# Optimization experiments

Measured on AMD Instinct MI355X. Metric: run time of the kernel, lower is better.

## Reference

```python
import jax, jax.numpy as jnp
import numpy as np

F = 16          # features
C = 128         # context features
H = 256         # conditioner hidden
L = 8           # coupling layers
K = 8           # spline bins
TB = 3.0        # tail bound
T = F // 2      # transform features per layer (8)
PDIM = 3 * K - 1  # params per transformed feature (23), tails='linear'
MIN_W = MIN_H = MIN_D = 1e-3
B = 65536


def _feature_split(layer):
    ev = np.arange(0, F, 2)
    od = np.arange(1, F, 2)
    tr, idn = (ev, od) if layer % 2 == 0 else (od, ev)  # mask>0 => transform
    inv = np.argsort(np.concatenate([idn, tr]))
    return idn, tr, inv


def _rq_spline(x, uw, uh, ud):
    """Monotonic rational-quadratic spline with linear tails (nflows semantics).
    x: [B,T]; uw/uh: [B,T,K]; ud: [B,T,K-1]. Returns (y, logabsdet) per element."""
    const = np.log(np.expm1(1.0 - MIN_D))  # pad value so boundary derivative == 1
    ud = jnp.pad(ud, ((0, 0), (0, 0), (1, 1)), constant_values=const)  # [B,T,K+1]
    inside = (x >= -TB) & (x <= TB)
    xs = jnp.clip(x, -TB, TB)

    w = jax.nn.softmax(uw, axis=-1)
    w = MIN_W + (1.0 - MIN_W * K) * w
    cw = jnp.pad(jnp.cumsum(w, -1), ((0, 0), (0, 0), (1, 0)))
    cw = 2.0 * TB * cw - TB
    cw = cw.at[..., 0].set(-TB).at[..., -1].set(TB)
    w = cw[..., 1:] - cw[..., :-1]

    d = MIN_D + jax.nn.softplus(ud)  # [B,T,K+1]

    h = jax.nn.softmax(uh, axis=-1)
    h = MIN_H + (1.0 - MIN_H * K) * h
    ch = jnp.pad(jnp.cumsum(h, -1), ((0, 0), (0, 0), (1, 0)))
    ch = 2.0 * TB * ch - TB
    ch = ch.at[..., 0].set(-TB).at[..., -1].set(TB)
    h = ch[..., 1:] - ch[..., :-1]

    # bin search on cumulative widths (forward direction)
    idx = jnp.clip(jnp.sum((xs[..., None] >= cw).astype(jnp.int32), -1) - 1, 0, K - 1)
    g = lambda a: jnp.take_along_axis(a, idx[..., None], axis=-1)[..., 0]

    x0, bw = g(cw[..., :K]), g(w)
    y0, bh = g(ch[..., :K]), g(h)
    delta = g(h / w)
    d0, d1 = g(d[..., :K]), g(d[..., 1:])

    th = (xs - x0) / bw
    th1m = th * (1.0 - th)
    num = bh * (delta * th * th + d0 * th1m)
    den = delta + (d0 + d1 - 2.0 * delta) * th1m
    y = y0 + num / den
    dnum = delta * delta * (d1 * th * th + 2.0 * delta * th1m + d0 * (1.0 - th) ** 2)
    ld = jnp.log(dnum) - 2.0 * jnp.log(den)
    return jnp.where(inside, y, x), jnp.where(inside, ld, 0.0)


def setup_inputs() -> dict:
    key = jax.random.key(0)
    ks = jax.random.split(key, 8)
    inputs = jax.random.normal(ks[0], (B, F), jnp.float32)
    context = jax.random.normal(ks[1], (B, C), jnp.float32)
    s = lambda k, shape, fan: jax.random.normal(k, shape, jnp.float32) / np.sqrt(fan)
    W1 = s(ks[2], (L, T + C, H), T + C)
    b1 = jnp.zeros((L, H), jnp.float32)
    W2 = s(ks[3], (L, H, H), H)
    b2 = jnp.zeros((L, H), jnp.float32)
    W3 = s(ks[4], (L, H, T * PDIM), H)
    b3 = jnp.zeros((L, T * PDIM), jnp.float32)
    rng = np.random.default_rng(0)  # fixed-at-init RandomPermutation buffers
    perms = jnp.asarray(np.stack([rng.permutation(F) for _ in range(L - 1)]), jnp.int32)
    return dict(inputs=inputs, context=context, W1=W1, b1=b1, W2=W2, b2=b2,
                W3=W3, b3=b3, perms=perms)


def reference(inputs, context, W1, b1, W2, b2, W3, b3, perms):
    x = jnp.clip(inputs, -1.0, 1.0)
    logdet = jnp.zeros(x.shape[0], x.dtype)
    for i in range(L):
        idn, tr, inv = _feature_split(i)
        xi = x[:, idn]
        xt = x[:, tr]
        hdn = jax.nn.relu(jnp.concatenate([xi, context], -1) @ W1[i] + b1[i])
        hdn = jax.nn.relu(hdn @ W2[i] + b2[i])
        p = (hdn @ W3[i] + b3[i]).reshape(-1, T, PDIM)
        yt, ld = _rq_spline(xt, p[..., :K], p[..., K:2 * K], p[..., 2 * K:])
        x = jnp.concatenate([xi, yt], -1)[:, inv]
        logdet = logdet + jnp.sum(ld, -1)
        if i < L - 1:
            x = x[:, perms[i]]
    return jnp.clip(x, -1.0, 1.0), logdet
```

## Files before the change

kernel.cpp:

```cpp
#include <hip/hip_runtime.h>
#include <math.h>

#define BATCH 65536
#define FDIM 16
#define CDIM 128
#define HDIM 256
#define NL 8
#define KBINS 8
#define TDIM 8
#define PD 23
#define TBV 3.0f
#define K1 160
#define N3 184
#define N3P 192
#define PSTR 197
#define MR 64
#define XSTR 40

typedef _Float16 f16;
typedef __attribute__((ext_vector_type(8))) _Float16 f16x8;
typedef __attribute__((ext_vector_type(4))) float f32x4;

__global__ __launch_bounds__(256)
void conv_w1_kernel(const float* __restrict__ W1,
                    f16* __restrict__ Wh, f16* __restrict__ Wl) {
    int idx = blockIdx.x * 256 + threadIdx.x;
    if (idx >= NL * HDIM * K1) return;
    int l = idx / (HDIM * K1);
    int rem = idx - l * (HDIM * K1);
    int n = rem / K1;
    int k = rem - n * K1;
    int row = (k < 128) ? (8 + k) : ((k < 136) ? (k - 128) : -1);
    float v = (row >= 0) ? W1[((size_t)l * 136 + row) * HDIM + n] : 0.f;
    f16 hv = (f16)v;
    Wh[idx] = hv; Wl[idx] = (f16)(v - (float)hv);
}

__global__ __launch_bounds__(256)
void conv_w2_kernel(const float* __restrict__ W2,
                    f16* __restrict__ Wh, f16* __restrict__ Wl) {
    int idx = blockIdx.x * 256 + threadIdx.x;
    if (idx >= NL * HDIM * HDIM) return;
    int l = idx / (HDIM * HDIM);
    int rem = idx - l * (HDIM * HDIM);
    int n = rem >> 8;
    int k = rem & 255;
    float v = W2[((size_t)l * HDIM + k) * HDIM + n];
    f16 hv = (f16)v;
    Wh[idx] = hv; Wl[idx] = (f16)(v - (float)hv);
}

__global__ __launch_bounds__(256)
void conv_w3_kernel(const float* __restrict__ W3,
                    f16* __restrict__ Wh, f16* __restrict__ Wl) {
    int idx = blockIdx.x * 256 + threadIdx.x;
    if (idx >= NL * N3P * HDIM) return;
    int l = idx / (N3P * HDIM);
    int rem = idx - l * (N3P * HDIM);
    int n = rem >> 8;
    int k = rem & 255;
    float v = (n < N3) ? W3[((size_t)l * HDIM + k) * N3 + n] : 0.f;
    f16 hv = (f16)v;
    Wh[idx] = hv; Wl[idx] = (f16)(v - (float)hv);
}

__global__ __launch_bounds__(256)
void conv_ctx_kernel(const float* __restrict__ ctx,
                     f16* __restrict__ ch, f16* __restrict__ cl) {
    size_t idx = ((size_t)blockIdx.x * 256 + threadIdx.x) * 4;
    if (idx >= (size_t)BATCH * CDIM) return;
    float4 v = *(const float4*)&ctx[idx];
    f16 h;
    h = (f16)v.x; ch[idx + 0] = h; cl[idx + 0] = (f16)(v.x - (float)h);
    h = (f16)v.y; ch[idx + 1] = h; cl[idx + 1] = (f16)(v.y - (float)h);
    h = (f16)v.z; ch[idx + 2] = h; cl[idx + 2] = (f16)(v.z - (float)h);
    h = (f16)v.w; ch[idx + 3] = h; cl[idx + 3] = (f16)(v.w - (float)h);
}

__device__ __forceinline__ float softplusf(float v) {
    return fmaxf(v, 0.f) + log1pf(expf(-fabsf(v)));
}

__device__ __forceinline__ void gld16(const f16* src, f16* dst) {
    __builtin_amdgcn_global_load_lds(
        (const __attribute__((address_space(1))) unsigned int*)src,
        (__attribute__((address_space(3))) unsigned int*)dst, 16, 0, 0);
}

template<int N> __device__ __forceinline__ void vmw() {
    asm volatile("s_waitcnt vmcnt(%0)" :: "n"(N) : "memory");
}
__device__ __forceinline__ void barr() {
    __builtin_amdgcn_s_barrier();
    __builtin_amdgcn_sched_barrier(0);
}
__device__ __forceinline__ void lgkm_bar() {
    asm volatile("s_waitcnt lgkmcnt(0)" ::: "memory");
    __builtin_amdgcn_s_barrier();
    __builtin_amdgcn_sched_barrier(0);
}

__global__ __launch_bounds__(512, 1)
void flow_kernel(const float* __restrict__ in,
                 const f16* __restrict__ ctxh, const f16* __restrict__ ctxl,
                 const f16* __restrict__ W1h, const f16* __restrict__ W1l,
                 const f16* __restrict__ W2h, const f16* __restrict__ W2l,
                 const f16* __restrict__ W3h, const f16* __restrict__ W3l,
                 const float* __restrict__ b1, const float* __restrict__ b2,
                 const float* __restrict__ b3, const int* __restrict__ perms,
                 float* __restrict__ out) {
    __shared__ __align__(16) char arena[131072];
    __shared__ __align__(16) f16 sXi[2][MR * XSTR];
    __shared__ float sX[2][MR][17];
    __shared__ float sY[MR][9];
    __shared__ float sLd[MR][9];
    __shared__ float sLdet[MR];
    __shared__ float sBias[768];
    __shared__ int   sPerm[(NL - 1) * FDIM];

    f16* sH = (f16*)arena;
    float* sP = (float*)arena;

    const int tid = threadIdx.x;
    const int lane = tid & 63;
    const int w = tid >> 6;
    const int lr = lane & 15, lh = lane >> 4;
    const int bid = blockIdx.x;
    const int wgid = (bid & 7) * 32 + (bid >> 3);
    const int wcol0 = w * 32;
    const int bxor = (lh ^ (lr & 3)) << 4;

    char* const wbuf = arena + 32768 + w * 12288;

    auto stageB = [&](const f16* Wh, const f16* Wl, int b, int kt, int KD) {
        char* dst = wbuf + b * 4096;
        #pragma unroll
        for (int ii = 0; ii < 2; ++ii) {
            int si = ii * 64 + lane;
            int c = si >> 2, seg = si & 3;
            const f16* sh = Wh + (size_t)(wcol0 + c) * KD + kt * 32 + (seg ^ (c & 3)) * 8;
            const f16* sl = Wl + (size_t)(wcol0 + c) * KD + kt * 32 + (seg ^ (c & 3)) * 8;
            gld16(sh, (f16*)(dst + ii * 1024 + lane * 16));
            gld16(sl, (f16*)(dst + 2048 + ii * 1024 + lane * 16));
        }
    };

    for (int rb = 0; rb < 4; ++rb) {
        const int rbase = (rb * 256 + wgid) * MR;
        lgkm_bar();

        {
            int r = tid >> 3, c2 = (tid & 7) * 2;
            float2 v = *(const float2*)&in[(size_t)(rbase + r) * FDIM + c2];
            sX[0][r][c2 + 0] = fminf(fmaxf(v.x, -1.f), 1.f);
            sX[0][r][c2 + 1] = fminf(fmaxf(v.y, -1.f), 1.f);
        }
        if (tid < MR) sLdet[tid] = 0.f;
        if (rb == 0 && tid < (NL - 1) * FDIM) sPerm[tid] = perms[tid];

        int cur = 0;
        for (int l = 0; l < NL; ++l) {
            lgkm_bar();

            {
                float bv1 = (tid < 256) ? b1[l * HDIM + tid]
                                        : b2[l * HDIM + (tid - 256)];
                float bv3 = b3[l * N3 + (tid < N3 ? tid : N3 - 1)];
                sBias[tid] = bv1;
                if (tid < N3) sBias[512 + tid] = bv3;
            }
            if (tid < MR) {
                int r = tid, off = 1 - (l & 1);
                #pragma unroll
                for (int k = 0; k < 8; ++k) {
                    float v = sX[cur][r][2 * k + off];
                    f16 hv = (f16)v;
                    sXi[0][r * XSTR + k] = hv;
                    sXi[1][r * XSTR + k] = (f16)(v - (float)hv);
                }
                #pragma unroll
                for (int k = 8; k < 32; ++k) {
                    sXi[0][r * XSTR + k] = (f16)0.f;
                    sXi[1][r * XSTR + k] = (f16)0.f;
                }
            }
            #pragma unroll
            for (int s = 0; s < 4; ++s) {
                int slot = s * 512 + tid;
                int p = slot >> 10, sp = slot & 1023;
                int row = sp >> 4, blk = sp & 15;
                const f16* src = (p ? ctxl : ctxh)
                               + (size_t)(rbase + row) * CDIM + (blk ^ (row & 7)) * 8;
                gld16(src, (f16*)(arena + slot * 16));
            }
            const f16* W1hL = W1h + (size_t)l * HDIM * K1;
            const f16* W1lL = W1l + (size_t)l * HDIM * K1;
            const f16* W2hL = W2h + (size_t)l * HDIM * HDIM;
            const f16* W2lL = W2l + (size_t)l * HDIM * HDIM;
            const f16* W3hL = W3h + (size_t)l * N3P * HDIM;
            const f16* W3lL = W3l + (size_t)l * N3P * HDIM;
            stageB(W1hL, W1lL, 0, 0, K1);
            stageB(W1hL, W1lL, 1, 1, K1);
            vmw<8>();
            lgkm_bar();

            f32x4 acc[4][2];
            #pragma unroll
            for (int i = 0; i < 4; ++i)
                #pragma unroll
                for (int j = 0; j < 2; ++j) acc[i][j] = (f32x4){0.f, 0.f, 0.f, 0.f};
            #pragma unroll
            for (int kt = 0; kt < 5; ++kt) {
                if (kt < 3) stageB(W1hL, W1lL, (kt + 2) % 3, kt + 2, K1);
                if (kt < 3) vmw<8>(); else if (kt == 3) vmw<4>(); else vmw<0>();
                f16x8 ah[4], al[4];
                if (kt < 4) {
                    #pragma unroll
                    for (int i = 0; i < 4; ++i) {
                        int row = i * 16 + lr;
                        int byo = row * 256 + ((kt * 64 + lh * 16) ^ ((row & 7) << 4));
                        ah[i] = *(const f16x8*)(arena + byo);
                        al[i] = *(const f16x8*)(arena + 16384 + byo);
                    }
                } else {
                    #pragma unroll
                    for (int i = 0; i < 4; ++i) {
                        int row = i * 16 + lr;
                        ah[i] = *(const f16x8*)&sXi[0][row * XSTR + lh * 8];
                        al[i] = *(const f16x8*)&sXi[1][row * XSTR + lh * 8];
                    }
                }
                const char* bb = wbuf + (kt % 3) * 4096;
                __builtin_amdgcn_s_setprio(1);
                #pragma unroll
                for (int j = 0; j < 2; ++j) {
                    int cb = (j * 16 + lr) * 64 + bxor;
                    f16x8 bh = *(const f16x8*)(bb + cb);
                    f16x8 bl = *(const f16x8*)(bb + 2048 + cb);
                    #pragma unroll
                    for (int i = 0; i < 4; ++i) {
                        acc[i][j] = __builtin_amdgcn_mfma_f32_16x16x32_f16(ah[i], bh, acc[i][j], 0, 0, 0);
                        acc[i][j] = __builtin_amdgcn_mfma_f32_16x16x32_f16(ah[i], bl, acc[i][j], 0, 0, 0);
                        acc[i][j] = __builtin_amdgcn_mfma_f32_16x16x32_f16(al[i], bh, acc[i][j], 0, 0, 0);
                    }
                }
                __builtin_amdgcn_s_setprio(0);
            }
            barr();
            #pragma unroll
            for (int j = 0; j < 2; ++j) {
                int col = wcol0 + j * 16 + lr;
                float bv = sBias[col];
                #pragma unroll
                for (int i = 0; i < 4; ++i)
                    #pragma unroll
                    for (int q = 0; q < 4; ++q) {
                        float v = fmaxf(acc[i][j][q] + bv, 0.f);
                        int row = i * 16 + lh * 4 + q;
                        int e = ((row << 8) + col) ^ ((row & 7) << 3);
                        sH[e] = (f16)v;
                    }
            }
            stageB(W2hL, W2lL, 0, 0, HDIM);
            stageB(W2hL, W2lL, 1, 1, HDIM);
            lgkm_bar();

            #pragma unroll
            for (int i = 0; i < 4; ++i)
                #pragma unroll
                for (int j = 0; j < 2; ++j) acc[i][j] = (f32x4){0.f, 0.f, 0.f, 0.f};
            #pragma unroll
            for (int kt = 0; kt < 8; ++kt) {
                if (kt < 6) stageB(W2hL, W2lL, (kt + 2) % 3, kt + 2, HDIM);
                if (kt < 6) vmw<8>(); else if (kt == 6) vmw<4>(); else vmw<0>();
                int k0 = kt * 32 + lh * 8;
                f16x8 ah[4];
                #pragma unroll
                for (int i = 0; i < 4; ++i) {
                    int row = i * 16 + lr;
                    int e = ((row << 8) + k0) ^ ((row & 7) << 3);
                    ah[i] = *(const f16x8*)&sH[e];
                }
                const char* bb = wbuf + (kt % 3) * 4096;
                __builtin_amdgcn_s_setprio(1);
                #pragma unroll
                for (int j = 0; j < 2; ++j) {
                    int cb = (j * 16 + lr) * 64 + bxor;
                    f16x8 bh = *(const f16x8*)(bb + cb);
                    f16x8 bl = *(const f16x8*)(bb + 2048 + cb);
                    #pragma unroll
                    for (int i = 0; i < 4; ++i) {
                        acc[i][j] = __builtin_amdgcn_mfma_f32_16x16x32_f16(ah[i], bh, acc[i][j], 0, 0, 0);
                        acc[i][j] = __builtin_amdgcn_mfma_f32_16x16x32_f16(ah[i], bl, acc[i][j], 0, 0, 0);
                    }
                }
                __builtin_amdgcn_s_setprio(0);
            }
            barr();
            #pragma unroll
            for (int j = 0; j < 2; ++j) {
                int col = wcol0 + j * 16 + lr;
                float bv = sBias[256 + col];
                #pragma unroll
                for (int i = 0; i < 4; ++i)
                    #pragma unroll
                    for (int q = 0; q < 4; ++q) {
                        float v = fmaxf(acc[i][j][q] + bv, 0.f);
                        int row = i * 16 + lh * 4 + q;
                        int e = ((row << 8) + col) ^ ((row & 7) << 3);
                        sH[e] = (f16)v;
                    }
            }
            if (w < 6) {
                stageB(W3hL, W3lL, 0, 0, HDIM);
                stageB(W3hL, W3lL, 1, 1, HDIM);
            }
            lgkm_bar();

            f32x4 acc3[4][2];
            #pragma unroll
            for (int i = 0; i < 4; ++i)
                #pragma unroll
                for (int j = 0; j < 2; ++j) acc3[i][j] = (f32x4){0.f, 0.f, 0.f, 0.f};
            if (w < 6) {
                #pragma unroll
                for (int kt = 0; kt < 8; ++kt) {
                    if (kt < 6) stageB(W3hL, W3lL, (kt + 2) % 3, kt + 2, HDIM);
                    if (kt < 6) vmw<8>(); else if (kt == 6) vmw<4>(); else vmw<0>();
                    int k0 = kt * 32 + lh * 8;
                    f16x8 ah[4];
                    #pragma unroll
                    for (int i = 0; i < 4; ++i) {
                        int row = i * 16 + lr;
                        int e = ((row << 8) + k0) ^ ((row & 7) << 3);
                        ah[i] = *(const f16x8*)&sH[e];
                    }
                    const char* bb = wbuf + (kt % 3) * 4096;
                    __builtin_amdgcn_s_setprio(1);
                    #pragma unroll
                    for (int j = 0; j < 2; ++j) {
                        int cb = (j * 16 + lr) * 64 + bxor;
                        f16x8 bh = *(const f16x8*)(bb + cb);
                        f16x8 bl = *(const f16x8*)(bb + 2048 + cb);
                        #pragma unroll
                        for (int i = 0; i < 4; ++i) {
                            acc3[i][j] = __builtin_amdgcn_mfma_f32_16x16x32_f16(ah[i], bh, acc3[i][j], 0, 0, 0);
                            acc3[i][j] = __builtin_amdgcn_mfma_f32_16x16x32_f16(ah[i], bl, acc3[i][j], 0, 0, 0);
                        }
                    }
                    __builtin_amdgcn_s_setprio(0);
                }
            }
            barr();
            if (w < 6) {
                #pragma unroll
                for (int j = 0; j < 2; ++j) {
                    int col = wcol0 + j * 16 + lr;
                    float bv = (col < N3) ? sBias[512 + col] : 0.f;
                    #pragma unroll
                    for (int i = 0; i < 4; ++i)
                        #pragma unroll
                        for (int q = 0; q < 4; ++q) {
                            int row = i * 16 + lh * 4 + q;
                            sP[row * PSTR + col] = acc3[i][j][q] + bv;
                        }
                }
            }
            lgkm_bar();

            {
                int r = tid & 63, t = tid >> 6;
                float xin = sX[cur][r][2 * t + (l & 1)];
                const float* pp = &sP[r * PSTR + t * PD];
                bool inside = (xin >= -TBV) && (xin <= TBV);
                float xs = fminf(fmaxf(xin, -TBV), TBV);

                float e0, e1, e2, e3, e4, e5, e6, e7;
                {
                    float a0 = pp[0], a1 = pp[1], a2 = pp[2], a3 = pp[3];
                    float a4 = pp[4], a5 = pp[5], a6 = pp[6], a7 = pp[7];
                    float m = fmaxf(fmaxf(fmaxf(a0, a1), fmaxf(a2, a3)),
                                    fmaxf(fmaxf(a4, a5), fmaxf(a6, a7)));
                    e0 = expf(a0 - m); e1 = expf(a1 - m); e2 = expf(a2 - m); e3 = expf(a3 - m);
                    e4 = expf(a4 - m); e5 = expf(a5 - m); e6 = expf(a6 - m); e7 = expf(a7 - m);
                }
                float swv = ((e0 + e1) + (e2 + e3)) + ((e4 + e5) + (e6 + e7));
                float cwc = (1.f - 0.001f * KBINS) / swv;
                float x0 = -TBV, x1 = TBV;
                int idx = 0;
                bool done = false;
                {
                    float cs = 0.f;
                    float ee[7] = {e0, e1, e2, e3, e4, e5, e6};
                    #pragma unroll
                    for (int k = 0; k < 7; ++k) {
                        cs += 0.001f + cwc * ee[k];
                        float nxt = 2.f * TBV * cs - TBV;
                        bool ge = (xs >= nxt);
                        x0 = ge ? nxt : x0;
                        idx += ge ? 1 : 0;
                        x1 = (!ge && !done) ? nxt : x1;
                        done = done || !ge;
                    }
                }
                float y0 = -TBV, y1 = TBV;
                {
                    float a0 = pp[8], a1 = pp[9], a2 = pp[10], a3 = pp[11];
                    float a4 = pp[12], a5 = pp[13], a6 = pp[14], a7 = pp[15];
                    float m = fmaxf(fmaxf(fmaxf(a0, a1), fmaxf(a2, a3)),
                                    fmaxf(fmaxf(a4, a5), fmaxf(a6, a7)));
                    float f0 = expf(a0 - m), f1 = expf(a1 - m), f2 = expf(a2 - m), f3 = expf(a3 - m);
                    float f4 = expf(a4 - m), f5 = expf(a5 - m), f6 = expf(a6 - m), f7 = expf(a7 - m);
                    float shv = ((f0 + f1) + (f2 + f3)) + ((f4 + f5) + (f6 + f7));
                    float chc = (1.f - 0.001f * KBINS) / shv;
                    float cs = 0.f;
                    float ff[7] = {f0, f1, f2, f3, f4, f5, f6};
                    #pragma unroll
                    for (int k = 0; k < 7; ++k) {
                        cs += 0.001f + chc * ff[k];
                        float nxt = 2.f * TBV * cs - TBV;
                        y0 = (k < idx) ? nxt : y0;
                        y1 = (k == idx) ? nxt : y1;
                    }
                }
                float udm = pp[16 + (idx > 0 ? idx - 1 : 0)];
                float udp = pp[16 + (idx < 7 ? idx : 6)];
                float d0 = (idx > 0) ? 0.001f + softplusf(udm) : 1.f;
                float d1 = (idx < 7) ? 0.001f + softplusf(udp) : 1.f;

                float bw = x1 - x0, bh2 = y1 - y0;
                float delta = bh2 / bw;
                float th = (xs - x0) / bw;
                float th1m = th * (1.f - th);
                float num = bh2 * (delta * th * th + d0 * th1m);
                float den = delta + (d0 + d1 - 2.f * delta) * th1m;
                float y = y0 + num / den;
                float omth = 1.f - th;
                float dnum = delta * delta * (d1 * th * th + 2.f * delta * th1m + d0 * omth * omth);
                float ldv = logf(dnum) - 2.f * logf(den);
                sY[r][t] = inside ? y : xin;
                sLd[r][t] = inside ? ldv : 0.f;
            }
            lgkm_bar();

            {
                int r = tid >> 3, f0 = (tid & 7) * 2;
                if (l < NL - 1) {
                    #pragma unroll
                    for (int ff = 0; ff < 2; ++ff) {
                        int f = f0 + ff;
                        int g = sPerm[l * FDIM + f];
                        float v = ((g & 1) == (l & 1)) ? sY[r][g >> 1] : sX[cur][r][g];
                        sX[cur ^ 1][r][f] = v;
                    }
                    if (f0 == 0) {
                        float s = 0.f;
                        #pragma unroll
                        for (int t = 0; t < 8; ++t) s += sLd[r][t];
                        sLdet[r] += s;
                    }
                } else {
                    float ov[2];
                    #pragma unroll
                    for (int ff = 0; ff < 2; ++ff) {
                        int f = f0 + ff;
                        float v = ((f & 1) == (l & 1)) ? sY[r][f >> 1] : sX[cur][r][f];
                        ov[ff] = fminf(fmaxf(v, -1.f), 1.f);
                    }
                    float2 o = {ov[0], ov[1]};
                    *(float2*)&out[(size_t)(rbase + r) * FDIM + f0] = o;
                    if (f0 == 0) {
                        float s = 0.f;
                        #pragma unroll
                        for (int t = 0; t < 8; ++t) s += sLd[r][t];
                        out[(size_t)BATCH * FDIM + rbase + r] = sLdet[r] + s;
                    }
                }
            }
            cur ^= 1;
        }
    }
}

extern "C" void kernel_launch(void* const* d_in, const int* in_sizes, int n_in,
                              void* d_out, int out_size, void* d_ws, size_t ws_size,
                              hipStream_t stream) {
    (void)in_sizes; (void)n_in; (void)out_size; (void)ws_size;
    const float* inputs  = (const float*)d_in[0];
    const float* context = (const float*)d_in[1];
    const float* W1 = (const float*)d_in[2];
    const float* b1 = (const float*)d_in[3];
    const float* W2 = (const float*)d_in[4];
    const float* b2 = (const float*)d_in[5];
    const float* W3 = (const float*)d_in[6];
    const float* b3 = (const float*)d_in[7];
    const int*   perms = (const int*)d_in[8];
    float* out = (float*)d_out;

    f16* W1h = (f16*)d_ws;
    f16* W1l = W1h + (size_t)NL * HDIM * K1;
    f16* W2h = W1l + (size_t)NL * HDIM * K1;
    f16* W2l = W2h + (size_t)NL * HDIM * HDIM;
    f16* W3h = W2l + (size_t)NL * HDIM * HDIM;
    f16* W3l = W3h + (size_t)NL * N3P * HDIM;
    f16* ctxh = W3l + (size_t)NL * N3P * HDIM;
    f16* ctxl = ctxh + (size_t)BATCH * CDIM;

    int n1 = NL * HDIM * K1;
    conv_w1_kernel<<<(n1 + 255) / 256, 256, 0, stream>>>(W1, W1h, W1l);
    int n2 = NL * HDIM * HDIM;
    conv_w2_kernel<<<(n2 + 255) / 256, 256, 0, stream>>>(W2, W2h, W2l);
    int n3 = NL * N3P * HDIM;
    conv_w3_kernel<<<(n3 + 255) / 256, 256, 0, stream>>>(W3, W3h, W3l);
    int nc = BATCH * CDIM / 4;
    conv_ctx_kernel<<<(nc + 255) / 256, 256, 0, stream>>>(context, ctxh, ctxl);

    flow_kernel<<<256, 512, 0, stream>>>(
        inputs, ctxh, ctxl, W1h, W1l, W2h, W2l, W3h, W3l,
        b1, b2, b3, perms, out);
}
```

Baseline: 587.5 us.

## Double-buffer weight staging, hoist context load, rebalance layer-3 columns across all waves

Gives context, weight staging and hidden activations their own LDS buffers, so context is loaded once per row block instead of once per layer. Weight tiles move from a triple-buffered prefetch to a double buffer that is refilled right after its MFMAs, with an lgkmcnt wait in front. The last GEMM's 192 columns are spread over all 8 waves (32 or 16 each) instead of 6 waves taking 32 and 2 sitting idle. The barrier after the first GEMM is removed. The shorter prefetch distance may expose more global latency, and the new LDS layout changes occupancy and bank behaviour.

```diff
diff --git a/kernel.cpp b/kernel.cpp
--- a/kernel.cpp
+++ b/kernel.cpp
@@ -90,6 +90,9 @@
 template<int N> __device__ __forceinline__ void vmw() {
     asm volatile("s_waitcnt vmcnt(%0)" :: "n"(N) : "memory");
 }
+__device__ __forceinline__ void lgkmw() {
+    asm volatile("s_waitcnt lgkmcnt(0)" ::: "memory");
+}
 __device__ __forceinline__ void barr() {
     __builtin_amdgcn_s_barrier();
     __builtin_amdgcn_sched_barrier(0);
@@ -109,7 +112,9 @@
                  const float* __restrict__ b1, const float* __restrict__ b2,
                  const float* __restrict__ b3, const int* __restrict__ perms,
                  float* __restrict__ out) {
-    __shared__ __align__(16) char arena[131072];
+    __shared__ __align__(16) f16 sCtx[16384];
+    __shared__ __align__(16) char warena[65536];
+    __shared__ __align__(16) f16 sH[16384];
     __shared__ __align__(16) f16 sXi[2][MR * XSTR];
     __shared__ float sX[2][MR][17];
     __shared__ float sY[MR][9];
@@ -118,8 +123,7 @@
     __shared__ float sBias[768];
     __shared__ int   sPerm[(NL - 1) * FDIM];
 
-    f16* sH = (f16*)arena;
-    float* sP = (float*)arena;
+    float* sP = (float*)warena;
 
     const int tid = threadIdx.x;
     const int lane = tid & 63;
@@ -128,20 +132,24 @@
     const int bid = blockIdx.x;
     const int wgid = (bid & 7) * 32 + (bid >> 3);
     const int wcol0 = w * 32;
+    const int wc3 = (w < 4) ? w * 32 : 128 + (w - 4) * 16;
     const int bxor = (lh ^ (lr & 3)) << 4;
 
-    char* const wbuf = arena + 32768 + w * 12288;
-
-    auto stageB = [&](const f16* Wh, const f16* Wl, int b, int kt, int KD) {
+    char* const wbuf = warena + w * 8192;
+
+    auto stageB = [&](const f16* Wh, const f16* Wl, int b, int kt, int KD,
+                      int colBase, int NC) {
         char* dst = wbuf + b * 4096;
         #pragma unroll
         for (int ii = 0; ii < 2; ++ii) {
-            int si = ii * 64 + lane;
-            int c = si >> 2, seg = si & 3;
-            const f16* sh = Wh + (size_t)(wcol0 + c) * KD + kt * 32 + (seg ^ (c & 3)) * 8;
-            const f16* sl = Wl + (size_t)(wcol0 + c) * KD + kt * 32 + (seg ^ (c & 3)) * 8;
-            gld16(sh, (f16*)(dst + ii * 1024 + lane * 16));
-            gld16(sl, (f16*)(dst + 2048 + ii * 1024 + lane * 16));
+            if (ii * 16 < NC) {
+                int si = ii * 64 + lane;
+                int c = si >> 2, seg = si & 3;
+                const f16* sh = Wh + (size_t)(colBase + c) * KD + kt * 32 + (seg ^ (c & 3)) * 8;
+                const f16* sl = Wl + (size_t)(colBase + c) * KD + kt * 32 + (seg ^ (c & 3)) * 8;
+                gld16(sh, (f16*)(dst + ii * 1024 + lane * 16));
+                gld16(sl, (f16*)(dst + NC * 64 + ii * 1024 + lane * 16));
+            }
         }
     };
 
@@ -158,6 +166,16 @@
         if (tid < MR) sLdet[tid] = 0.f;
         if (rb == 0 && tid < (NL - 1) * FDIM) sPerm[tid] = perms[tid];
 
+        #pragma unroll
+        for (int s = 0; s < 4; ++s) {
+            int slot = s * 512 + tid;
+            int p = slot >> 10, sp = slot & 1023;
+            int row = sp >> 4, blk = sp & 15;
+            const f16* src = (p ? ctxl : ctxh)
+                           + (size_t)(rbase + row) * CDIM + (blk ^ (row & 7)) * 8;
+            gld16(src, &sCtx[slot * 8]);
+        }
+
         int cur = 0;
         for (int l = 0; l < NL; ++l) {
             lgkm_bar();
@@ -184,24 +202,14 @@
                     sXi[1][r * XSTR + k] = (f16)0.f;
                 }
             }
-            #pragma unroll
-            for (int s = 0; s < 4; ++s) {
-                int slot = s * 512 + tid;
-                int p = slot >> 10, sp = slot & 1023;
-                int row = sp >> 4, blk = sp & 15;
-                const f16* src = (p ? ctxl : ctxh)
-                               + (size_t)(rbase + row) * CDIM + (blk ^ (row & 7)) * 8;
-                gld16(src, (f16*)(arena + slot * 16));
-            }
             const f16* W1hL = W1h + (size_t)l * HDIM * K1;
             const f16* W1lL = W1l + (size_t)l * HDIM * K1;
             const f16* W2hL = W2h + (size_t)l * HDIM * HDIM;
             const f16* W2lL = W2l + (size_t)l * HDIM * HDIM;
             const f16* W3hL = W3h + (size_t)l * N3P * HDIM;
             const f16* W3lL = W3l + (size_t)l * N3P * HDIM;
-            stageB(W1hL, W1lL, 0, 0, K1);
-            stageB(W1hL, W1lL, 1, 1, K1);
-            vmw<8>();
+            stageB(W1hL, W1lL, 0, 0, K1, wcol0, 32);
+            stageB(W1hL, W1lL, 1, 1, K1, wcol0, 32);
             lgkm_bar();
 
             f32x4 acc[4][2];
@@ -211,16 +219,15 @@
                 for (int j = 0; j < 2; ++j) acc[i][j] = (f32x4){0.f, 0.f, 0.f, 0.f};
             #pragma unroll
             for (int kt = 0; kt < 5; ++kt) {
-                if (kt < 3) stageB(W1hL, W1lL, (kt + 2) % 3, kt + 2, K1);
-                if (kt < 3) vmw<8>(); else if (kt == 3) vmw<4>(); else vmw<0>();
+                if (kt < 4) vmw<4>(); else vmw<0>();
                 f16x8 ah[4], al[4];
                 if (kt < 4) {
                     #pragma unroll
                     for (int i = 0; i < 4; ++i) {
                         int row = i * 16 + lr;
                         int byo = row * 256 + ((kt * 64 + lh * 16) ^ ((row & 7) << 4));
-                        ah[i] = *(const f16x8*)(arena + byo);
-                        al[i] = *(const f16x8*)(arena + 16384 + byo);
+                        ah[i] = *(const f16x8*)((const char*)sCtx + byo);
+                        al[i] = *(const f16x8*)((const char*)sCtx + 16384 + byo);
                     }
                 } else {
                     #pragma unroll
@@ -230,7 +237,7 @@
                         al[i] = *(const f16x8*)&sXi[1][row * XSTR + lh * 8];
                     }
                 }
-                const char* bb = wbuf + (kt % 3) * 4096;
+                const char* bb = wbuf + (kt & 1) * 4096;
                 __builtin_amdgcn_s_setprio(1);
                 #pragma unroll
                 for (int j = 0; j < 2; ++j) {
@@ -245,8 +252,11 @@
                     }
                 }
                 __builtin_amdgcn_s_setprio(0);
-            }
-            barr();
+                if (kt + 2 < 5) {
+                    lgkmw();
+                    stageB(W1hL, W1lL, kt & 1, kt + 2, K1, wcol0, 32);
+                }
+            }
             #pragma unroll
             for (int j = 0; j < 2; ++j) {
                 int col = wcol0 + j * 16 + lr;
@@ -261,8 +271,8 @@
                         sH[e] = (f16)v;
                     }
             }
-            stageB(W2hL, W2lL, 0, 0, HDIM);
-            stageB(W2hL, W2lL, 1, 1, HDIM);
+            stageB(W2hL, W2lL, 0, 0, HDIM, wcol0, 32);
+            stageB(W2hL, W2lL, 1, 1, HDIM, wcol0, 32);
             lgkm_bar();
 
             #pragma unroll
@@ -271,8 +281,7 @@
                 for (int j = 0; j < 2; ++j) acc[i][j] = (f32x4){0.f, 0.f, 0.f, 0.f};
             #pragma unroll
             for (int kt = 0; kt < 8; ++kt) {
-                if (kt < 6) stageB(W2hL, W2lL, (kt + 2) % 3, kt + 2, HDIM);
-                if (kt < 6) vmw<8>(); else if (kt == 6) vmw<4>(); else vmw<0>();
+                if (kt < 7) vmw<4>(); else vmw<0>();
                 int k0 = kt * 32 + lh * 8;
                 f16x8 ah[4];
                 #pragma unroll
@@ -281,7 +290,7 @@
                     int e = ((row << 8) + k0) ^ ((row & 7) << 3);
                     ah[i] = *(const f16x8*)&sH[e];
                 }
-                const char* bb = wbuf + (kt % 3) * 4096;
+                const char* bb = wbuf + (kt & 1) * 4096;
                 __builtin_amdgcn_s_setprio(1);
                 #pragma unroll
                 for (int j = 0; j < 2; ++j) {
@@ -295,6 +304,10 @@
                     }
                 }
                 __builtin_amdgcn_s_setprio(0);
+                if (kt + 2 < 8) {
+                    lgkmw();
+                    stageB(W2hL, W2lL, kt & 1, kt + 2, HDIM, wcol0, 32);
+                }
             }
             barr();
             #pragma unroll
@@ -311,9 +324,10 @@
                         sH[e] = (f16)v;
                     }
             }
-            if (w < 6) {
-                stageB(W3hL, W3lL, 0, 0, HDIM);
-                stageB(W3hL, W3lL, 1, 1, HDIM);
+            {
+                const int NC3 = (w < 4) ? 32 : 16;
+                stageB(W3hL, W3lL, 0, 0, HDIM, wc3, NC3);
+                stageB(W3hL, W3lL, 1, 1, HDIM, wc3, NC3);
             }
             lgkm_bar();
 
@@ -322,11 +336,13 @@
             for (int i = 0; i < 4; ++i)
                 #pragma unroll
                 for (int j = 0; j < 2; ++j) acc3[i][j] = (f32x4){0.f, 0.f, 0.f, 0.f};
-            if (w < 6) {
+            {
+                const int NC3 = (w < 4) ? 32 : 16;
+                const int nc64 = NC3 * 64;
                 #pragma unroll
                 for (int kt = 0; kt < 8; ++kt) {
-                    if (kt < 6) stageB(W3hL, W3lL, (kt + 2) % 3, kt + 2, HDIM);
-                    if (kt < 6) vmw<8>(); else if (kt == 6) vmw<4>(); else vmw<0>();
+                    if (kt < 7) { if (w < 4) vmw<4>(); else vmw<2>(); }
+                    else vmw<0>();
                     int k0 = kt * 32 + lh * 8;
                     f16x8 ah[4];
                     #pragma unroll
@@ -335,34 +351,55 @@
                         int e = ((row << 8) + k0) ^ ((row & 7) << 3);
                         ah[i] = *(const f16x8*)&sH[e];
                     }
-                    const char* bb = wbuf + (kt % 3) * 4096;
+                    const char* bb = wbuf + (kt & 1) * 4096;
                     __builtin_amdgcn_s_setprio(1);
-                    #pragma unroll
-                    for (int j = 0; j < 2; ++j) {
-                        int cb = (j * 16 + lr) * 64 + bxor;
+                    {
+                        int cb = lr * 64 + bxor;
                         f16x8 bh = *(const f16x8*)(bb + cb);
-                        f16x8 bl = *(const f16x8*)(bb + 2048 + cb);
+                        f16x8 bl = *(const f16x8*)(bb + nc64 + cb);
                         #pragma unroll
                         for (int i = 0; i < 4; ++i) {
-                            acc3[i][j] = __builtin_amdgcn_mfma_f32_16x16x32_f16(ah[i], bh, acc3[i][j], 0, 0, 0);
-                            acc3[i][j] = __builtin_amdgcn_mfma_f32_16x16x32_f16(ah[i], bl, acc3[i][j], 0, 0, 0);
+                            acc3[i][0] = __builtin_amdgcn_mfma_f32_16x16x32_f16(ah[i], bh, acc3[i][0], 0, 0, 0);
+                            acc3[i][0] = __builtin_amdgcn_mfma_f32_16x16x32_f16(ah[i], bl, acc3[i][0], 0, 0, 0);
                         }
                     }
+                    if (w < 4) {
+                        int cb = (16 + lr) * 64 + bxor;
+                        f16x8 bh = *(const f16x8*)(bb + cb);
+                        f16x8 bl = *(const f16x8*)(bb + nc64 + cb);
+                        #pragma unroll
+                        for (int i = 0; i < 4; ++i) {
+                            acc3[i][1] = __builtin_amdgcn_mfma_f32_16x16x32_f16(ah[i], bh, acc3[i][1], 0, 0, 0);
+                            acc3[i][1] = __builtin_amdgcn_mfma_f32_16x16x32_f16(ah[i], bl, acc3[i][1], 0, 0, 0);
+                        }
+                    }
                     __builtin_amdgcn_s_setprio(0);
+                    if (kt + 2 < 8) {
+                        lgkmw();
+                        stageB(W3hL, W3lL, kt & 1, kt + 2, HDIM, wc3, NC3);
+                    }
                 }
             }
             barr();
-            if (w < 6) {
-                #pragma unroll
-                for (int j = 0; j < 2; ++j) {
-                    int col = wcol0 + j * 16 + lr;
-                    float bv = (col < N3) ? sBias[512 + col] : 0.f;
+            {
+                int col = wc3 + lr;
+                float bv = (col < N3) ? sBias[512 + col] : 0.f;
+                #pragma unroll
+                for (int i = 0; i < 4; ++i)
+                    #pragma unroll
+                    for (int q = 0; q < 4; ++q) {
+                        int row = i * 16 + lh * 4 + q;
+                        sP[row * PSTR + col] = acc3[i][0][q] + bv;
+                    }
+                if (w < 4) {
+                    int col1 = wc3 + 16 + lr;
+                    float bv1 = sBias[512 + col1];
                     #pragma unroll
                     for (int i = 0; i < 4; ++i)
                         #pragma unroll
                         for (int q = 0; q < 4; ++q) {
                             int row = i * 16 + lh * 4 + q;
-                            sP[row * PSTR + col] = acc3[i][j][q] + bv;
+                            sP[row * PSTR + col1] = acc3[i][1][q] + bv1;
                         }
                 }
             }
```

New measurement: 529.7 us. 9.8% less time.
